# Performance work log

Measured on AMD Instinct MI355X. Metric: run time of the kernel, lower is better.

## Reference

```python
import jax, jax.numpy as jnp
import numpy as np


def setup_inputs() -> dict:
    key = jax.random.key(0)
    ks = jax.random.split(key, 6)
    b, l, d, n, r = 2, 2048, 512, 64, 32
    x = jax.random.normal(ks[0], (b, l, d), dtype=jnp.float32)
    # x_proj: Linear(d, r + 2n, bias=False) -> weight (r+2n, d)
    W_xproj = jax.random.normal(ks[1], (r + 2 * n, d), dtype=jnp.float32) / np.sqrt(d)
    # dt_proj: Linear(r, d, bias=True)
    W_dt = jax.random.normal(ks[2], (d, r), dtype=jnp.float32) / np.sqrt(r)
    b_dt = jax.random.normal(ks[3], (d,), dtype=jnp.float32) * 0.01
    # A_log = log(repeat(arange(1, n+1), 'n -> d n'))
    A_log = jnp.log(jnp.broadcast_to(jnp.arange(1, n + 1, dtype=jnp.float32), (d, n)))
    D = jnp.ones((d,), dtype=jnp.float32)
    return {"x": x, "W_xproj": W_xproj, "W_dt": W_dt, "b_dt": b_dt, "A_log": A_log, "D": D}


def _s6_forward(x, W_xproj, W_dt, b_dt, A_log, D):
    d, n = A_log.shape
    r = W_dt.shape[1]
    A = -jnp.exp(A_log)                               # (d, n)
    x_dbl = jnp.einsum('bld,ed->ble', x, W_xproj)     # (b, l, r+2n)
    delta_r = x_dbl[..., :r]
    B = x_dbl[..., r:r + n]                           # (b, l, n)
    C = x_dbl[..., r + n:]                            # (b, l, n)
    delta = jax.nn.softplus(jnp.einsum('blr,dr->bld', delta_r, W_dt) + b_dt)  # (b, l, d)
    # discretize
    deltaA = jnp.exp(jnp.einsum('bld,dn->bldn', delta, A))        # (b, l, d, n)
    deltaB_u = jnp.einsum('bld,bln,bld->bldn', delta, B, x)       # (b, l, d, n)
    bsz = x.shape[0]
    h0 = jnp.zeros((bsz, d, n), dtype=x.dtype)

    def step(h, inp):
        dA_t, dBu_t, C_t = inp                        # (b,d,n), (b,d,n), (b,n)
        h = dA_t * h + dBu_t
        y_t = jnp.einsum('bdn,bn->bd', h, C_t)
        return h, y_t

    xs = (jnp.moveaxis(deltaA, 1, 0), jnp.moveaxis(deltaB_u, 1, 0), jnp.moveaxis(C, 1, 0))
    _, ys = jax.lax.scan(step, h0, xs)                # ys: (l, b, d)
    y = jnp.moveaxis(ys, 0, 1)                        # (b, l, d)
    return y + x * D


def reference(x, W_xproj, W_dt, b_dt, A_log, D):
    return _s6_forward(x, W_xproj, W_dt, b_dt, A_log, D)
```

## Files before the change

### kernel.cpp

```cpp
#include <hip/hip_runtime.h>
#include <cstdint>

#define Bsz 2
#define Lsz 2048
#define Dm  512
#define Nst 64
#define Rr  32
#define Ee  160
#define NCHUNK 32
#define CLEN   64
#define L2E 1.44269504f
#define LN2 0.69314718f

typedef __bf16  bf16x8 __attribute__((ext_vector_type(8)));
typedef float   f32x4  __attribute__((ext_vector_type(4)));
typedef unsigned short u16x8 __attribute__((ext_vector_type(8)));

__device__ __forceinline__ float rdlane(float v, int l) {
    return __int_as_float(__builtin_amdgcn_readlane(__float_as_int(v), l));
}
__device__ __forceinline__ float fexp2(float x) { return __builtin_amdgcn_exp2f(x); }
__device__ __forceinline__ float flog2(float x) { return __builtin_amdgcn_logf(x); }

__global__ __launch_bounds__(256) void kcast(const float* __restrict__ in,
                                             unsigned short* __restrict__ outp,
                                             int n8) {
    int gid = blockIdx.x * 256 + threadIdx.x;
    if (gid >= n8) return;
    const float4* ip = reinterpret_cast<const float4*>(in) + (size_t)gid * 2;
    float4 v0 = ip[0], v1 = ip[1];
    float vv[8] = {v0.x, v0.y, v0.z, v0.w, v1.x, v1.y, v1.z, v1.w};
    u16x8 r;
    #pragma unroll
    for (int j = 0; j < 8; ++j) {
        uint32_t u = __float_as_uint(vv[j]);
        u += 0x7FFFu + ((u >> 16) & 1u);
        r[j] = (unsigned short)(u >> 16);
    }
    *reinterpret_cast<u16x8*>(outp + (size_t)gid * 8) = r;
}

__global__ __launch_bounds__(256) void k1_mfma(const unsigned short* __restrict__ xbf,
                                               const unsigned short* __restrict__ wbf,
                                               float* __restrict__ xdbl) {
    const int tid = threadIdx.x;
    const int wv = tid >> 6, lane = tid & 63;
    const int ng = blockIdx.x % 10, mg = blockIdx.x / 10;
    const int m0 = mg * 64 + wv * 16;
    const int n0 = ng * 16;
    const int ra = lane & 15, kg = lane >> 4;
    const unsigned short* ap = xbf + (size_t)(m0 + ra) * Dm + kg * 8;
    const unsigned short* bp = wbf + (size_t)(n0 + ra) * Dm + kg * 8;
    f32x4 acc = {0.f, 0.f, 0.f, 0.f};
    #pragma unroll
    for (int ks = 0; ks < 16; ++ks) {
        bf16x8 a = *reinterpret_cast<const bf16x8*>(ap + ks * 32);
        bf16x8 b = *reinterpret_cast<const bf16x8*>(bp + ks * 32);
        acc = __builtin_amdgcn_mfma_f32_16x16x32_bf16(a, b, acc, 0, 0, 0);
    }
    float* dp = xdbl + (size_t)(m0 + kg * 4) * Ee + n0 + ra;
    dp[0]      = acc[0];
    dp[Ee]     = acc[1];
    dp[2 * Ee] = acc[2];
    dp[3 * Ee] = acc[3];
}

__global__ __launch_bounds__(256) void k2_delta(const float* __restrict__ xdbl,
                                                const float* __restrict__ x,
                                                const float* __restrict__ Wdt,
                                                const float* __restrict__ bdt,
                                                float* __restrict__ delta_t,
                                                float* __restrict__ du_t,
                                                float* __restrict__ sumdl) {
    __shared__ float dr[64][33];
    __shared__ float wd[64][32];
    __shared__ float pt[64][65];
    const int tid = threadIdx.x;
    const int lt = blockIdx.x & 31;
    const int dt = (blockIdx.x >> 5) & 7;
    const int b  = blockIdx.x >> 8;
    const int l0 = lt * 64, d0 = dt * 64;

    for (int i = tid; i < 512; i += 256) {
        int l = i >> 3, j4 = i & 7;
        const float4 v = *reinterpret_cast<const float4*>(
            xdbl + (size_t)(b * Lsz + l0 + l) * Ee + j4 * 4);
        dr[l][j4 * 4 + 0] = v.x; dr[l][j4 * 4 + 1] = v.y;
        dr[l][j4 * 4 + 2] = v.z; dr[l][j4 * 4 + 3] = v.w;
    }
    for (int i = tid; i < 512; i += 256) {
        int dd = i >> 3, j4 = i & 7;
        *reinterpret_cast<float4*>(&wd[dd][j4 * 4]) =
            *reinterpret_cast<const float4*>(Wdt + (size_t)(d0 + dd) * Rr + j4 * 4);
    }
    __syncthreads();

    const int w = tid >> 6, lane = tid & 63;
    float drr[32];
    #pragma unroll
    for (int j = 0; j < 32; ++j) drr[j] = dr[lane][j];

    float xv[16];
    {
        const float* xp = x + (size_t)(b * Lsz + l0 + lane) * Dm + d0 + w * 16;
        #pragma unroll
        for (int q = 0; q < 4; ++q) {
            float4 v = reinterpret_cast<const float4*>(xp)[q];
            xv[q*4] = v.x; xv[q*4+1] = v.y; xv[q*4+2] = v.z; xv[q*4+3] = v.w;
        }
    }

    float dl[16];
    #pragma unroll
    for (int i = 0; i < 16; ++i) {
        int dd = w * 16 + i;
        float z = bdt[d0 + dd];
        const float4* wr = reinterpret_cast<const float4*>(&wd[dd][0]);
        #pragma unroll
        for (int j4 = 0; j4 < 8; ++j4) {
            float4 wv = wr[j4];
            z = fmaf(drr[j4*4+0], wv.x, z);
            z = fmaf(drr[j4*4+1], wv.y, z);
            z = fmaf(drr[j4*4+2], wv.z, z);
            z = fmaf(drr[j4*4+3], wv.w, z);
        }
        float t = fexp2(-fabsf(z) * L2E);
        dl[i] = fmaxf(z, 0.f) + flog2(1.f + t) * LN2;
    }

    #pragma unroll
    for (int i = 0; i < 16; ++i) pt[w * 16 + i][lane] = dl[i];
    __syncthreads();
    for (int i = tid; i < 4096; i += 256) {
        int dd = i >> 6, ll = i & 63;
        delta_t[((size_t)(b * Dm + d0 + dd)) * Lsz + l0 + ll] = pt[dd][ll];
    }
    if (tid < 64) {
        float s = 0.f;
        #pragma unroll 16
        for (int q = 0; q < 64; ++q) s += pt[tid][q];
        sumdl[(size_t)(b * Dm + d0 + tid) * NCHUNK + lt] = s;
    }
    __syncthreads();
    #pragma unroll
    for (int i = 0; i < 16; ++i) pt[w * 16 + i][lane] = dl[i] * xv[i];
    __syncthreads();
    for (int i = tid; i < 4096; i += 256) {
        int dd = i >> 6, ll = i & 63;
        du_t[((size_t)(b * Dm + d0 + dd)) * Lsz + l0 + ll] = pt[dd][ll];
    }
}

__global__ __launch_bounds__(256, 4) void k3a(const float* __restrict__ delta_t,
                                              const float* __restrict__ du_t,
                                              const float* __restrict__ xdbl,
                                              const float* __restrict__ Alog,
                                              float* __restrict__ hf) {
    __shared__ float Bs[64][64];
    const int tid = threadIdx.x;
    const int w = __builtin_amdgcn_readfirstlane(tid >> 6);
    const int lane = tid & 63;
    const int c   = blockIdx.x & 31;
    const int grp = blockIdx.x >> 5;
    const int chan0 = grp * 32 + w * 8;
    const int b = chan0 >> 9;
    const int t0 = c * CLEN;
    const float* __restrict__ xb0 = xdbl + ((size_t)b * Lsz + t0) * Ee;
    for (int i = tid; i < 1024; i += 256) {
        int row = i >> 4, q = i & 15;
        float4 v = *reinterpret_cast<const float4*>(xb0 + row * Ee + Rr + q * 4);
        *reinterpret_cast<float4*>(&Bs[row][q * 4]) = v;
    }
    float A2[8], h[8], dreg[8], ureg[8];
    #pragma unroll
    for (int ch = 0; ch < 8; ++ch) {
        const int cc = chan0 + ch;
        A2[ch] = -expf(Alog[(size_t)(cc & 511) * Nst + lane]) * L2E;
        dreg[ch] = delta_t[(size_t)cc * Lsz + t0 + lane];
        ureg[ch] = du_t   [(size_t)cc * Lsz + t0 + lane];
        h[ch] = 0.f;
    }
    __syncthreads();
    #pragma unroll 8
    for (int j = 0; j < CLEN; ++j) {
        float Bv = Bs[j][lane];
        #pragma unroll
        for (int ch = 0; ch < 8; ++ch) {
            float sd = rdlane(dreg[ch], j);
            float su = rdlane(ureg[ch], j);
            h[ch] = fmaf(fexp2(sd * A2[ch]), h[ch], su * Bv);
        }
    }
    #pragma unroll
    for (int ch = 0; ch < 8; ++ch)
        hf[((size_t)(chan0 + ch) * NCHUNK + c) * Nst + lane] = h[ch];
}

__global__ __launch_bounds__(256) void k3b(const float* __restrict__ Alog,
                                           const float* __restrict__ sumdl,
                                           float* __restrict__ hf) {
    const int tid = threadIdx.x;
    const int w = tid >> 6, lane = tid & 63;
    const int chan = blockIdx.x * 4 + w;
    const int d = chan & 511;
    const float A2 = -expf(Alog[(size_t)d * Nst + lane]) * L2E;
    const float sv = sumdl[chan * NCHUNK + (lane & 31)];
    const size_t base = (size_t)chan * NCHUNK * Nst + lane;
    float hv[8], nx[8];
    #pragma unroll
    for (int i = 0; i < 8; ++i) hv[i] = hf[base + i * Nst];
    float h0 = 0.f;
    for (int g = 0; g < 4; ++g) {
        if (g < 3) {
            #pragma unroll
            for (int i = 0; i < 8; ++i) nx[i] = hf[base + ((g + 1) * 8 + i) * Nst];
        }
        #pragma unroll
        for (int i = 0; i < 8; ++i) {
            const int c = g * 8 + i;
            float P = fexp2(A2 * rdlane(sv, c));
            hf[base + c * Nst] = h0;
            h0 = fmaf(P, h0, hv[i]);
        }
        #pragma unroll
        for (int i = 0; i < 8; ++i) hv[i] = nx[i];
    }
}

__global__ __launch_bounds__(256, 3) void k3c(const float* __restrict__ delta_t,
                                              const float* __restrict__ du_t,
                                              const float* __restrict__ xdbl,
                                              const float* __restrict__ Alog,
                                              const float* __restrict__ h0s,
                                              const float* __restrict__ x,
                                              const float* __restrict__ Dv,
                                              float* __restrict__ out) {
    __shared__ float BC[32][128];
    __shared__ float part[4][16][65];
    __shared__ float ystage[4][8][66];
    const int tid = threadIdx.x;
    const int w = __builtin_amdgcn_readfirstlane(tid >> 6);
    const int lane = tid & 63;
    const int c   = blockIdx.x & 31;
    const int grp = blockIdx.x >> 5;
    const int chan0 = grp * 32 + w * 8;
    const int b = chan0 >> 9;
    const int t0 = c * CLEN;
    const float* __restrict__ xb0 = xdbl + ((size_t)b * Lsz + t0) * Ee;

    float A2[8], h[8], dreg[8], ureg[8];
    #pragma unroll
    for (int ch = 0; ch < 8; ++ch) {
        const int cc = chan0 + ch;
        A2[ch] = -expf(Alog[(size_t)(cc & 511) * Nst + lane]) * L2E;
        dreg[ch] = delta_t[(size_t)cc * Lsz + t0 + lane];
        ureg[ch] = du_t   [(size_t)cc * Lsz + t0 + lane];
        h[ch] = h0s[((size_t)cc * NCHUNK + c) * Nst + lane];
    }
    const int r = lane & 15, seg = lane >> 4;

    #pragma unroll
    for (int half = 0; half < 2; ++half) {
        if (half) __syncthreads();
        for (int i = tid; i < 1024; i += 256) {
            int row = i >> 5, q4 = i & 31;
            float4 v = *reinterpret_cast<const float4*>(
                xb0 + (half * 32 + row) * Ee + Rr + q4 * 4);
            *reinterpret_cast<float4*>(&BC[row][q4 * 4]) = v;
        }
        __syncthreads();
        #pragma unroll
        for (int g2 = 0; g2 < 16; ++g2) {
            #pragma unroll
            for (int jj = 0; jj < 2; ++jj) {
                const int tt = g2 * 2 + jj;
                const int t  = half * 32 + tt;
                float Bv = BC[tt][lane];
                float Cv = BC[tt][64 + lane];
                #pragma unroll
                for (int ch = 0; ch < 8; ++ch) {
                    float sd = rdlane(dreg[ch], t);
                    float su = rdlane(ureg[ch], t);
                    h[ch] = fmaf(fexp2(sd * A2[ch]), h[ch], su * Bv);
                    part[w][ch * 2 + jj][lane] = h[ch] * Cv;
                }
            }
            float v = 0.f;
            #pragma unroll
            for (int q = 0; q < 16; ++q) v += part[w][r][seg * 16 + q];
            v += __shfl_xor(v, 16);
            v += __shfl_xor(v, 32);
            if (lane < 16) ystage[w][r >> 1][half * 32 + g2 * 2 + (r & 1)] = v;
        }
    }
    __syncthreads();
    const int d0 = (grp * 32) & 511;
    for (int i = tid; i < 2048; i += 256) {
        int t = i >> 5, dd = i & 31;
        size_t gi = ((size_t)(b * Lsz + t0 + t)) * Dm + d0 + dd;
        out[gi] = ystage[dd >> 3][dd & 7][t] + x[gi] * Dv[d0 + dd];
    }
}

extern "C" void kernel_launch(void* const* d_in, const int* in_sizes, int n_in,
                              void* d_out, int out_size, void* d_ws, size_t ws_size,
                              hipStream_t stream) {
    const float* x    = (const float*)d_in[0];
    const float* Wxp  = (const float*)d_in[1];
    const float* Wdt  = (const float*)d_in[2];
    const float* bdt  = (const float*)d_in[3];
    const float* Alog = (const float*)d_in[4];
    const float* Dv   = (const float*)d_in[5];
    float* out = (float*)d_out;

    float* ws = (float*)d_ws;
    float*          xdbl    = ws;
    unsigned short* xbf     = (unsigned short*)(ws + 655360);
    unsigned short* wbf     = (unsigned short*)(ws + 1703936);
    float*          delta_t = ws + 1744896;
    float*          du_t    = ws + 3842048;
    float*          hf      = ws + 5939200;
    float*          sumdl   = ws + 8036352;

    hipLaunchKernelGGL(kcast,   dim3(1024), dim3(256), 0, stream, x,   xbf, 262144);
    hipLaunchKernelGGL(kcast,   dim3(40),   dim3(256), 0, stream, Wxp, wbf, 10240);
    hipLaunchKernelGGL(k1_mfma, dim3(640),  dim3(256), 0, stream, xbf, wbf, xdbl);
    hipLaunchKernelGGL(k2_delta,dim3(512),  dim3(256), 0, stream, xdbl, x, Wdt, bdt, delta_t, du_t, sumdl);
    hipLaunchKernelGGL(k3a,     dim3(1024), dim3(256), 0, stream, delta_t, du_t, xdbl, Alog, hf);
    hipLaunchKernelGGL(k3b,     dim3(256),  dim3(256), 0, stream, Alog, sumdl, hf);
    hipLaunchKernelGGL(k3c,     dim3(1024), dim3(256), 0, stream, delta_t, du_t, xdbl, Alog, hf, x, Dv, out);
}
```

Before: 121.5 us.

## Fuse cast launches, halve k3a channels per wave, per-step y reduction in k3c

The two fp32-to-bf16 cast launches are merged into one kernel that dispatches on global thread index, removing one launch. k3a now handles 4 channels per wave instead of 8 and launches twice as many blocks, which raises parallelism for the chunk-local scan but loads the B tile from memory twice as often. k3c reduces h*C for every timestep rather than pairs of timesteps, using a smaller partial buffer and an extra shuffle, and its occupancy hint is raised from 3 to 4 blocks. Together these aim to cut launch overhead and improve latency hiding in the scan kernels, at the cost of more reduction passes and more LDS round trips in k3c.

```diff
diff --git a/kernel.cpp b/kernel.cpp
--- a/kernel.cpp
+++ b/kernel.cpp
@@ -22,12 +22,15 @@
 __device__ __forceinline__ float fexp2(float x) { return __builtin_amdgcn_exp2f(x); }
 __device__ __forceinline__ float flog2(float x) { return __builtin_amdgcn_logf(x); }
 
-__global__ __launch_bounds__(256) void kcast(const float* __restrict__ in,
-                                             unsigned short* __restrict__ outp,
-                                             int n8) {
+__global__ __launch_bounds__(256) void kcast2(const float* __restrict__ a,
+                                              unsigned short* __restrict__ oa, int na8,
+                                              const float* __restrict__ b,
+                                              unsigned short* __restrict__ ob, int nb8) {
     int gid = blockIdx.x * 256 + threadIdx.x;
-    if (gid >= n8) return;
-    const float4* ip = reinterpret_cast<const float4*>(in) + (size_t)gid * 2;
+    const float* in; unsigned short* op; int idx;
+    if (gid < na8) { in = a; op = oa; idx = gid; }
+    else { idx = gid - na8; if (idx >= nb8) return; in = b; op = ob; }
+    const float4* ip = reinterpret_cast<const float4*>(in) + (size_t)idx * 2;
     float4 v0 = ip[0], v1 = ip[1];
     float vv[8] = {v0.x, v0.y, v0.z, v0.w, v1.x, v1.y, v1.z, v1.w};
     u16x8 r;
@@ -37,7 +40,7 @@
         u += 0x7FFFu + ((u >> 16) & 1u);
         r[j] = (unsigned short)(u >> 16);
     }
-    *reinterpret_cast<u16x8*>(outp + (size_t)gid * 8) = r;
+    *reinterpret_cast<u16x8*>(op + (size_t)idx * 8) = r;
 }
 
 __global__ __launch_bounds__(256) void k1_mfma(const unsigned short* __restrict__ xbf,
@@ -151,12 +154,93 @@
     }
 }
 
-__global__ __launch_bounds__(256, 4) void k3a(const float* __restrict__ delta_t,
+__global__ __launch_bounds__(256) void k3a(const float* __restrict__ delta_t,
+                                           const float* __restrict__ du_t,
+                                           const float* __restrict__ xdbl,
+                                           const float* __restrict__ Alog,
+                                           float* __restrict__ hf) {
+    __shared__ float Bs[64][64];
+    const int tid = threadIdx.x;
+    const int w = __builtin_amdgcn_readfirstlane(tid >> 6);
+    const int lane = tid & 63;
+    const int c   = blockIdx.x & 31;
+    const int grp = blockIdx.x >> 5;
+    const int chan0 = grp * 16 + w * 4;
+    const int b = chan0 >> 9;
+    const int t0 = c * CLEN;
+    const float* __restrict__ xb0 = xdbl + ((size_t)b * Lsz + t0) * Ee;
+    for (int i = tid; i < 1024; i += 256) {
+        int row = i >> 4, q = i & 15;
+        float4 v = *reinterpret_cast<const float4*>(xb0 + row * Ee + Rr + q * 4);
+        *reinterpret_cast<float4*>(&Bs[row][q * 4]) = v;
+    }
+    float A2[4], h[4], dreg[4], ureg[4];
+    #pragma unroll
+    for (int ch = 0; ch < 4; ++ch) {
+        const int cc = chan0 + ch;
+        A2[ch] = -expf(Alog[(size_t)(cc & 511) * Nst + lane]) * L2E;
+        dreg[ch] = delta_t[(size_t)cc * Lsz + t0 + lane];
+        ureg[ch] = du_t   [(size_t)cc * Lsz + t0 + lane];
+        h[ch] = 0.f;
+    }
+    __syncthreads();
+    #pragma unroll 8
+    for (int j = 0; j < CLEN; ++j) {
+        float Bv = Bs[j][lane];
+        #pragma unroll
+        for (int ch = 0; ch < 4; ++ch) {
+            float sd = rdlane(dreg[ch], j);
+            float su = rdlane(ureg[ch], j);
+            h[ch] = fmaf(fexp2(sd * A2[ch]), h[ch], su * Bv);
+        }
+    }
+    #pragma unroll
+    for (int ch = 0; ch < 4; ++ch)
+        hf[((size_t)(chan0 + ch) * NCHUNK + c) * Nst + lane] = h[ch];
+}
+
+__global__ __launch_bounds__(256) void k3b(const float* __restrict__ Alog,
+                                           const float* __restrict__ sumdl,
+                                           float* __restrict__ hf) {
+    const int tid = threadIdx.x;
+    const int w = tid >> 6, lane = tid & 63;
+    const int chan = blockIdx.x * 4 + w;
+    const int d = chan & 511;
+    const float A2 = -expf(Alog[(size_t)d * Nst + lane]) * L2E;
+    const float sv = sumdl[chan * NCHUNK + (lane & 31)];
+    const size_t base = (size_t)chan * NCHUNK * Nst + lane;
+    float hv[8], nx[8];
+    #pragma unroll
+    for (int i = 0; i < 8; ++i) hv[i] = hf[base + i * Nst];
+    float h0 = 0.f;
+    for (int g = 0; g < 4; ++g) {
+        if (g < 3) {
+            #pragma unroll
+            for (int i = 0; i < 8; ++i) nx[i] = hf[base + ((g + 1) * 8 + i) * Nst];
+        }
+        #pragma unroll
+        for (int i = 0; i < 8; ++i) {
+            const int c = g * 8 + i;
+            float P = fexp2(A2 * rdlane(sv, c));
+            hf[base + c * Nst] = h0;
+            h0 = fmaf(P, h0, hv[i]);
+        }
+        #pragma unroll
+        for (int i = 0; i < 8; ++i) hv[i] = nx[i];
+    }
+}
+
+__global__ __launch_bounds__(256, 4) void k3c(const float* __restrict__ delta_t,
                                               const float* __restrict__ du_t,
                                               const float* __restrict__ xdbl,
                                               const float* __restrict__ Alog,
-                                              float* __restrict__ hf) {
-    __shared__ float Bs[64][64];
+                                              const float* __restrict__ h0s,
+                                              const float* __restrict__ x,
+                                              const float* __restrict__ Dv,
+                                              float* __restrict__ out) {
+    __shared__ float BC[32][128];
+    __shared__ float part[4][8][65];
+    __shared__ float ystage[4][8][66];
     const int tid = threadIdx.x;
     const int w = __builtin_amdgcn_readfirstlane(tid >> 6);
     const int lane = tid & 63;
@@ -166,87 +250,6 @@
     const int b = chan0 >> 9;
     const int t0 = c * CLEN;
     const float* __restrict__ xb0 = xdbl + ((size_t)b * Lsz + t0) * Ee;
-    for (int i = tid; i < 1024; i += 256) {
-        int row = i >> 4, q = i & 15;
-        float4 v = *reinterpret_cast<const float4*>(xb0 + row * Ee + Rr + q * 4);
-        *reinterpret_cast<float4*>(&Bs[row][q * 4]) = v;
-    }
-    float A2[8], h[8], dreg[8], ureg[8];
-    #pragma unroll
-    for (int ch = 0; ch < 8; ++ch) {
-        const int cc = chan0 + ch;
-        A2[ch] = -expf(Alog[(size_t)(cc & 511) * Nst + lane]) * L2E;
-        dreg[ch] = delta_t[(size_t)cc * Lsz + t0 + lane];
-        ureg[ch] = du_t   [(size_t)cc * Lsz + t0 + lane];
-        h[ch] = 0.f;
-    }
-    __syncthreads();
-    #pragma unroll 8
-    for (int j = 0; j < CLEN; ++j) {
-        float Bv = Bs[j][lane];
-        #pragma unroll
-        for (int ch = 0; ch < 8; ++ch) {
-            float sd = rdlane(dreg[ch], j);
-            float su = rdlane(ureg[ch], j);
-            h[ch] = fmaf(fexp2(sd * A2[ch]), h[ch], su * Bv);
-        }
-    }
-    #pragma unroll
-    for (int ch = 0; ch < 8; ++ch)
-        hf[((size_t)(chan0 + ch) * NCHUNK + c) * Nst + lane] = h[ch];
-}
-
-__global__ __launch_bounds__(256) void k3b(const float* __restrict__ Alog,
-                                           const float* __restrict__ sumdl,
-                                           float* __restrict__ hf) {
-    const int tid = threadIdx.x;
-    const int w = tid >> 6, lane = tid & 63;
-    const int chan = blockIdx.x * 4 + w;
-    const int d = chan & 511;
-    const float A2 = -expf(Alog[(size_t)d * Nst + lane]) * L2E;
-    const float sv = sumdl[chan * NCHUNK + (lane & 31)];
-    const size_t base = (size_t)chan * NCHUNK * Nst + lane;
-    float hv[8], nx[8];
-    #pragma unroll
-    for (int i = 0; i < 8; ++i) hv[i] = hf[base + i * Nst];
-    float h0 = 0.f;
-    for (int g = 0; g < 4; ++g) {
-        if (g < 3) {
-            #pragma unroll
-            for (int i = 0; i < 8; ++i) nx[i] = hf[base + ((g + 1) * 8 + i) * Nst];
-        }
-        #pragma unroll
-        for (int i = 0; i < 8; ++i) {
-            const int c = g * 8 + i;
-            float P = fexp2(A2 * rdlane(sv, c));
-            hf[base + c * Nst] = h0;
-            h0 = fmaf(P, h0, hv[i]);
-        }
-        #pragma unroll
-        for (int i = 0; i < 8; ++i) hv[i] = nx[i];
-    }
-}
-
-__global__ __launch_bounds__(256, 3) void k3c(const float* __restrict__ delta_t,
-                                              const float* __restrict__ du_t,
-                                              const float* __restrict__ xdbl,
-                                              const float* __restrict__ Alog,
-                                              const float* __restrict__ h0s,
-                                              const float* __restrict__ x,
-                                              const float* __restrict__ Dv,
-                                              float* __restrict__ out) {
-    __shared__ float BC[32][128];
-    __shared__ float part[4][16][65];
-    __shared__ float ystage[4][8][66];
-    const int tid = threadIdx.x;
-    const int w = __builtin_amdgcn_readfirstlane(tid >> 6);
-    const int lane = tid & 63;
-    const int c   = blockIdx.x & 31;
-    const int grp = blockIdx.x >> 5;
-    const int chan0 = grp * 32 + w * 8;
-    const int b = chan0 >> 9;
-    const int t0 = c * CLEN;
-    const float* __restrict__ xb0 = xdbl + ((size_t)b * Lsz + t0) * Ee;
 
     float A2[8], h[8], dreg[8], ureg[8];
     #pragma unroll
@@ -257,7 +260,7 @@
         ureg[ch] = du_t   [(size_t)cc * Lsz + t0 + lane];
         h[ch] = h0s[((size_t)cc * NCHUNK + c) * Nst + lane];
     }
-    const int r = lane & 15, seg = lane >> 4;
+    const int r8 = lane & 7, sg = lane >> 3;
 
     #pragma unroll
     for (int half = 0; half < 2; ++half) {
@@ -269,28 +272,25 @@
             *reinterpret_cast<float4*>(&BC[row][q4 * 4]) = v;
         }
         __syncthreads();
-        #pragma unroll
-        for (int g2 = 0; g2 < 16; ++g2) {
+        #pragma unroll 8
+        for (int tt = 0; tt < 32; ++tt) {
+            const int t = half * 32 + tt;
+            float Bv = BC[tt][lane];
+            float Cv = BC[tt][64 + lane];
             #pragma unroll
-            for (int jj = 0; jj < 2; ++jj) {
-                const int tt = g2 * 2 + jj;
-                const int t  = half * 32 + tt;
-                float Bv = BC[tt][lane];
-                float Cv = BC[tt][64 + lane];
-                #pragma unroll
-                for (int ch = 0; ch < 8; ++ch) {
-                    float sd = rdlane(dreg[ch], t);
-                    float su = rdlane(ureg[ch], t);
-                    h[ch] = fmaf(fexp2(sd * A2[ch]), h[ch], su * Bv);
-                    part[w][ch * 2 + jj][lane] = h[ch] * Cv;
-                }
+            for (int ch = 0; ch < 8; ++ch) {
+                float sd = rdlane(dreg[ch], t);
+                float su = rdlane(ureg[ch], t);
+                h[ch] = fmaf(fexp2(sd * A2[ch]), h[ch], su * Bv);
+                part[w][ch][lane] = h[ch] * Cv;
             }
             float v = 0.f;
             #pragma unroll
-            for (int q = 0; q < 16; ++q) v += part[w][r][seg * 16 + q];
+            for (int q = 0; q < 8; ++q) v += part[w][r8][sg * 8 + q];
+            v += __shfl_xor(v, 8);
             v += __shfl_xor(v, 16);
             v += __shfl_xor(v, 32);
-            if (lane < 16) ystage[w][r >> 1][half * 32 + g2 * 2 + (r & 1)] = v;
+            if (lane < 8) ystage[w][lane][t] = v;
         }
     }
     __syncthreads();
@@ -322,11 +322,10 @@
     float*          hf      = ws + 5939200;
     float*          sumdl   = ws + 8036352;
 
-    hipLaunchKernelGGL(kcast,   dim3(1024), dim3(256), 0, stream, x,   xbf, 262144);
-    hipLaunchKernelGGL(kcast,   dim3(40),   dim3(256), 0, stream, Wxp, wbf, 10240);
+    hipLaunchKernelGGL(kcast2,  dim3(1064), dim3(256), 0, stream, x, xbf, 262144, Wxp, wbf, 10240);
     hipLaunchKernelGGL(k1_mfma, dim3(640),  dim3(256), 0, stream, xbf, wbf, xdbl);
     hipLaunchKernelGGL(k2_delta,dim3(512),  dim3(256), 0, stream, xdbl, x, Wdt, bdt, delta_t, du_t, sumdl);
-    hipLaunchKernelGGL(k3a,     dim3(1024), dim3(256), 0, stream, delta_t, du_t, xdbl, Alog, hf);
+    hipLaunchKernelGGL(k3a,     dim3(2048), dim3(256), 0, stream, delta_t, du_t, xdbl, Alog, hf);
     hipLaunchKernelGGL(k3b,     dim3(256),  dim3(256), 0, stream, Alog, sumdl, hf);
     hipLaunchKernelGGL(k3c,     dim3(1024), dim3(256), 0, stream, delta_t, du_t, xdbl, Alog, hf, x, Dv, out);
 }
```

Result: no change. 121.0 us (-0.4%).
